# Optimization experiments

Measured on AMD Instinct MI355X. Metric: run time of the kernel, lower is better.

The kernel has to match this reference:

```python
import jax, jax.numpy as jnp
from jax import lax
import numpy as np

B, S, D, H, OUT = 32, 512, 512, 512, 256


def setup_inputs() -> dict:
    key = jax.random.key(0)
    ks = jax.random.split(key, 12)
    sc = 0.05
    return {
        "x": jax.random.normal(ks[0], (B, S, D), jnp.float32),
        "Wf0": jax.random.normal(ks[1], (D + H, H), jnp.float32) * sc,
        "bf0": jax.random.normal(ks[2], (H,), jnp.float32) * sc,
        "Wb0": jax.random.normal(ks[3], (D + H, H), jnp.float32) * sc,
        "bb0": jax.random.normal(ks[4], (H,), jnp.float32) * sc,
        "Wf1": jax.random.normal(ks[5], (3 * H, H), jnp.float32) * sc,
        "bf1": jax.random.normal(ks[6], (H,), jnp.float32) * sc,
        "Wb1": jax.random.normal(ks[7], (3 * H, H), jnp.float32) * sc,
        "bb1": jax.random.normal(ks[8], (H,), jnp.float32) * sc,
        "Wfc": jax.random.normal(ks[9], (2 * H, OUT), jnp.float32) * sc,
        "bfc": jax.random.normal(ks[10], (OUT,), jnp.float32) * sc,
    }


def _direction(xin, W, b, reverse):
    # xin: [B,S,Din]; W: [Din+H, H]. Split into input and hidden parts so the
    # big input projection is one GEMM; only h @ Wh stays in the scan.
    Din = xin.shape[-1]
    Wx, Wh = W[:Din], W[Din:]
    xw = jnp.einsum('bsd,dh->sbh', xin, Wx) + b  # [S,B,H]

    def step(h, xt):
        h = jnp.tanh(xt + h @ Wh)
        return h, h

    h0 = jnp.zeros((xin.shape[0], Wh.shape[1]), xin.dtype)
    h_last, ys = lax.scan(step, h0, xw, reverse=reverse)
    return h_last, jnp.transpose(ys, (1, 0, 2))  # [B,S,H]


def _bilayer(xin, Wf, bf, Wb, bb):
    h_f, out_f = _direction(xin, Wf, bf, reverse=False)
    h_b, out_b = _direction(xin, Wb, bb, reverse=True)
    return jnp.concatenate([out_f, out_b], axis=-1), h_f, h_b


def reference(x, Wf0, bf0, Wb0, bb0, Wf1, bf1, Wb1, bb1, Wfc, bfc):
    y0, hf0, hb0 = _bilayer(x, Wf0, bf0, Wb0, bb0)
    y1, hf1, hb1 = _bilayer(y0, Wf1, bf1, Wb1, bb1)
    seq_repr = jnp.concatenate([hf1, hb1], axis=-1)  # [B, 2H]
    logits = seq_repr @ Wfc + bfc
    final_hf = jnp.stack([hf0, hf1])  # [L,B,H]
    final_hb = jnp.stack([hb0, hb1])
    return logits, final_hf, final_hb
```

## Files before the change

kernel.cpp:

```cpp
#include <hip/hip_runtime.h>


typedef unsigned short u16;
typedef unsigned int u32;
typedef __attribute__((ext_vector_type(8))) short short8;
typedef __attribute__((ext_vector_type(4))) float f32x4;
typedef __attribute__((ext_vector_type(2))) unsigned int u32x2;

#define DEV static __device__ __forceinline__

DEV u16 f2bf(float f) {
  u32 u = __builtin_bit_cast(u32, f);
  u = (u + 0x7fffu + ((u >> 16) & 1u)) >> 16;
  return (u16)u;
}
DEV float bf2f(u16 h) { return __builtin_bit_cast(float, ((u32)h) << 16); }

DEV f32x4 MFMA(short8 a, short8 b, f32x4 c) {
  return __builtin_amdgcn_mfma_f32_16x16x32_bf16(a, b, c, 0, 0, 0);
}

DEV float fast_tanh(float x) {
  float e = exp2f(x * 2.885390082f);
  return 1.0f - 2.0f * __builtin_amdgcn_rcpf(e + 1.0f);
}

DEV short8 ld_b128_coh(const u16* p) {
  short8 r;
  asm volatile("global_load_dwordx4 %0, %1, off sc0 sc1" : "=v"(r) : "v"(p) : "memory");
  return r;
}
DEV short8 ld_b128_l2(const u16* p) {
  short8 r;
  asm volatile("global_load_dwordx4 %0, %1, off sc0" : "=v"(r) : "v"(p) : "memory");
  return r;
}
DEV f32x4 ld_f32x4_vm(const float* p) {
  f32x4 r;
  asm volatile("global_load_dwordx4 %0, %1, off" : "=v"(r) : "v"(p) : "memory");
  return r;
}
DEV u32 ld_u32_coh(const u32* p) {
  u32 r;
  asm volatile("global_load_dword %0, %1, off sc0 sc1\n\ts_waitcnt vmcnt(0)"
               : "=v"(r) : "v"(p) : "memory");
  return r;
}
DEV void st_b64_coh(u16* p, u32x2 v) {
  asm volatile("global_store_dwordx2 %0, %1, off sc0 sc1" :: "v"(p), "v"(v) : "memory");
}
DEV void st_b64_l2(u16* p, u32x2 v) {
  asm volatile("global_store_dwordx2 %0, %1, off sc0" :: "v"(p), "v"(v) : "memory");
}
DEV void st_u32_coh(u32* p, u32 v) {
  asm volatile("global_store_dword %0, %1, off sc0 sc1" :: "v"(p), "v"(v) : "memory");
}
DEV void vm_drain() { asm volatile("s_waitcnt vmcnt(0)" ::: "memory"); }

template<bool LOCAL>
DEV u32 tag_poll(u32* p) {
  u32 r; u32 z = 0;
  if (LOCAL)
    asm volatile("global_atomic_add %0, %1, %2, off sc0\n\ts_waitcnt vmcnt(0)"
                 : "=v"(r) : "v"(p), "v"(z) : "memory");
  else
    asm volatile("global_atomic_add %0, %1, %2, off sc0 sc1\n\ts_waitcnt vmcnt(0)"
                 : "=v"(r) : "v"(p), "v"(z) : "memory");
  return r;
}
template<bool LOCAL>
DEV void tag_post(u32* p) {
  u32 one = 1;
  if (LOCAL)
    asm volatile("global_atomic_add %0, %1, off" :: "v"(p), "v"(one) : "memory");
  else
    asm volatile("global_atomic_add %0, %1, off sc1" :: "v"(p), "v"(one) : "memory");
}

constexpr size_t OFF_CNT  = 0;
constexpr size_t OFF_MB   = 1024;
constexpr size_t OFF_WT0F = 32768;
constexpr size_t NE_WT0   = 512 * 1024;
constexpr size_t SZ_WT0   = NE_WT0 * 2 * 2;
constexpr size_t OFF_WT0B = OFF_WT0F + SZ_WT0;
constexpr size_t OFF_WT1F = OFF_WT0B + SZ_WT0;
constexpr size_t NE_WT1   = 512 * 1536;
constexpr size_t SZ_WT1   = NE_WT1 * 2 * 2;
constexpr size_t OFF_WT1B = OFF_WT1F + SZ_WT1;
constexpr size_t OFF_XWF  = OFF_WT1B + SZ_WT1;
constexpr size_t SZ_XW    = 16384ull * 512 * 4;
constexpr size_t OFF_XWB  = OFF_XWF + SZ_XW;
constexpr size_t OFF_Y0   = OFF_XWB + SZ_XW;
constexpr size_t SZ_Y0    = 16384ull * 1024 * 4;
constexpr size_t OFF_H    = OFF_Y0 + SZ_Y0;

DEV void phase_barrier(u32* c, u32 target) {
  __syncthreads();
  if (threadIdx.x == 0) {
    __hip_atomic_fetch_add(c, 1u, __ATOMIC_RELEASE, __HIP_MEMORY_SCOPE_AGENT);
    int spins = 0;
    while (__hip_atomic_load(c, __ATOMIC_RELAXED, __HIP_MEMORY_SCOPE_AGENT) < target) {
      __builtin_amdgcn_s_sleep(32);
      if (++spins > (1 << 20)) break;
    }
    __builtin_amdgcn_fence(__ATOMIC_ACQUIRE, "agent");
  }
  __syncthreads();
}

DEV void proj_phase(const float* __restrict__ A, bool perm, int bpitch, int bkoff, int K,
                    const u16* __restrict__ wfh, const u16* __restrict__ wfl,
                    const u16* __restrict__ wbh, const u16* __restrict__ wbl,
                    const float* __restrict__ biasF, const float* __restrict__ biasB,
                    float* __restrict__ Cf, float* __restrict__ Cb,
                    u16* aHi, u16* aLo, u16* bHi, u16* bLo) {
  const int tid = threadIdx.x;
  const int l = tid & 63, w = tid >> 6;
  const int lr = l & 15, lk = (l >> 4) * 8;
  const int wm = (w >> 1) * 64, wn = (w & 1) * 64;
  for (int t = blockIdx.x; t < 1024; t += 256) {
    const int dir = t >> 9, tile = t & 511;
    const int mbase = (tile >> 2) * 128, nbase = (tile & 3) * 128;
    const u16* bh_src = dir ? wbh : wfh;
    const u16* bl_src = dir ? wbl : wfl;
    const float* bias = dir ? biasB : biasF;
    float* C = dir ? Cb : Cf;
    f32x4 acc[4][4] = {};
    for (int kk = 0; kk < K; kk += 32) {
      {
        const int row = tid >> 1, half = tid & 1;
        const int r = mbase + row;
        const int srcRow = perm ? (((r & 31) << 9) + (r >> 5)) : r;
        const float* ap = A + (size_t)srcRow * K + kk + half * 16;
        f32x4 q0 = *(const f32x4*)(ap + 0);
        f32x4 q1 = *(const f32x4*)(ap + 4);
        f32x4 q2 = *(const f32x4*)(ap + 8);
        f32x4 q3 = *(const f32x4*)(ap + 12);
        short8 h0, l0, h1, l1;
        #pragma unroll
        for (int e = 0; e < 4; ++e) {
          { float v = q0[e]; u16 hv = f2bf(v); h0[e]   = (short)hv; l0[e]   = (short)f2bf(v - bf2f(hv)); }
          { float v = q1[e]; u16 hv = f2bf(v); h0[e+4] = (short)hv; l0[e+4] = (short)f2bf(v - bf2f(hv)); }
          { float v = q2[e]; u16 hv = f2bf(v); h1[e]   = (short)hv; l1[e]   = (short)f2bf(v - bf2f(hv)); }
          { float v = q3[e]; u16 hv = f2bf(v); h1[e+4] = (short)hv; l1[e+4] = (short)f2bf(v - bf2f(hv)); }
        }
        const int o = row * 40 + half * 16;
        *(short8*)&aHi[o] = h0; *(short8*)&aHi[o + 8] = h1;
        *(short8*)&aLo[o] = l0; *(short8*)&aLo[o + 8] = l1;
        const size_t bo = (size_t)(nbase + row) * bpitch + bkoff + kk + half * 16;
        *(short8*)&bHi[o]     = *(const short8*)&bh_src[bo];
        *(short8*)&bHi[o + 8] = *(const short8*)&bh_src[bo + 8];
        *(short8*)&bLo[o]     = *(const short8*)&bl_src[bo];
        *(short8*)&bLo[o + 8] = *(const short8*)&bl_src[bo + 8];
      }
      __syncthreads();
      short8 afh[4], afl[4], bfh[4], bfl[4];
      #pragma unroll
      for (int i = 0; i < 4; ++i) {
        afh[i] = *(short8*)&aHi[(wm + i * 16 + lr) * 40 + lk];
        afl[i] = *(short8*)&aLo[(wm + i * 16 + lr) * 40 + lk];
        bfh[i] = *(short8*)&bHi[(wn + i * 16 + lr) * 40 + lk];
        bfl[i] = *(short8*)&bLo[(wn + i * 16 + lr) * 40 + lk];
      }
      #pragma unroll
      for (int i = 0; i < 4; ++i)
        #pragma unroll
        for (int j = 0; j < 4; ++j) {
          acc[i][j] = MFMA(afh[i], bfh[j], acc[i][j]);
          acc[i][j] = MFMA(afh[i], bfl[j], acc[i][j]);
          acc[i][j] = MFMA(afl[i], bfh[j], acc[i][j]);
        }
      __syncthreads();
    }
    #pragma unroll
    for (int i = 0; i < 4; ++i)
      #pragma unroll
      for (int j = 0; j < 4; ++j) {
        const int gcol = nbase + wn + j * 16 + lr;
        const float bv = bias[gcol];
        #pragma unroll
        for (int rr = 0; rr < 4; ++rr) {
          const int grow = mbase + wm + i * 16 + (l >> 4) * 4 + rr;
          C[(size_t)grow * 512 + gcol] = acc[i][j][rr] + bv;
        }
      }
  }
}

template<bool LOCAL>
DEV void recurrence(bool fwd, const float* __restrict__ xw,
                    const u16* __restrict__ wtHi, const u16* __restrict__ wtLo,
                    int wpitch, int wkoff,
                    u16* __restrict__ hHi, u16* __restrict__ hLo,
                    float* __restrict__ y0, int ycol0,
                    u32* mb, int wgslot, float* red) {
  const int tid = threadIdx.x;
  const int l = tid & 63, w = tid >> 6;
  const int lr = l & 15, lk4 = l >> 4;
  const int c0 = wgslot * 32;
  short8 wfh[2][4], wfl[2][4];
  #pragma unroll
  for (int ct = 0; ct < 2; ++ct)
    #pragma unroll
    for (int ks = 0; ks < 4; ++ks) {
      const size_t o = (size_t)(c0 + ct * 16 + lr) * wpitch + wkoff + w * 128 + ks * 32 + lk4 * 8;
      wfh[ct][ks] = *(const short8*)&wtHi[o];
      wfl[ct][ks] = *(const short8*)&wtLo[o];
    }
  const int frow = (w & 1) * 16 + lr;
  const int fcb  = c0 + (w >> 1) * 16 + lk4 * 4;
  const u32 mySlot = (u32)(wgslot * 4 + w);
  u32* pollp = mb + wgslot * 64 + l;
  int budget = 1 << 22;
  for (int t = 0; t < 512; ++t) {
    const int s = fwd ? t : (511 - t);
    f32x4 xwv = ld_f32x4_vm(xw + (size_t)(s * 32 + frow) * 512 + fcb);
    if (t) {
      for (;;) {
        u32 v = tag_poll<LOCAL>(pollp);
        if (__all((int)(v >= (u32)t))) break;
        if (--budget < 0) break;
      }
    }
    const u16* hh = hHi + (t & 1) * 16384;
    const u16* hl = hLo + (t & 1) * 16384;
    u16* nhh = hHi + ((t & 1) ^ 1) * 16384;
    u16* nhl = hLo + ((t & 1) ^ 1) * 16384;
    short8 hfh0[4], hfl0[4], hfh1[4], hfl1[4];
    #pragma unroll
    for (int g = 0; g < 4; ++g) {
      const int k = w * 128 + g * 32 + lk4 * 8;
      if (LOCAL) {
        hfh0[g] = ld_b128_l2(&hh[lr * 512 + k]);
        hfl0[g] = ld_b128_l2(&hl[lr * 512 + k]);
        hfh1[g] = ld_b128_l2(&hh[(16 + lr) * 512 + k]);
        hfl1[g] = ld_b128_l2(&hl[(16 + lr) * 512 + k]);
      } else {
        hfh0[g] = ld_b128_coh(&hh[lr * 512 + k]);
        hfl0[g] = ld_b128_coh(&hl[lr * 512 + k]);
        hfh1[g] = ld_b128_coh(&hh[(16 + lr) * 512 + k]);
        hfl1[g] = ld_b128_coh(&hl[(16 + lr) * 512 + k]);
      }
    }
    f32x4 acc[2][2] = {};
    #pragma unroll
    for (int g = 0; g < 4; ++g) {
      if (g == 0)      asm volatile("s_waitcnt vmcnt(12)" ::: "memory");
      else if (g == 1) asm volatile("s_waitcnt vmcnt(8)"  ::: "memory");
      else if (g == 2) asm volatile("s_waitcnt vmcnt(4)"  ::: "memory");
      else             asm volatile("s_waitcnt vmcnt(0)"  ::: "memory");
      __builtin_amdgcn_sched_barrier(0);
      #pragma unroll
      for (int ct = 0; ct < 2; ++ct) {
        acc[ct][0] = MFMA(wfh[ct][g], hfh0[g], acc[ct][0]);
        acc[ct][0] = MFMA(wfh[ct][g], hfl0[g], acc[ct][0]);
        acc[ct][0] = MFMA(wfl[ct][g], hfh0[g], acc[ct][0]);
        acc[ct][1] = MFMA(wfh[ct][g], hfh1[g], acc[ct][1]);
        acc[ct][1] = MFMA(wfh[ct][g], hfl1[g], acc[ct][1]);
        acc[ct][1] = MFMA(wfl[ct][g], hfh1[g], acc[ct][1]);
      }
    }
    #pragma unroll
    for (int ct = 0; ct < 2; ++ct)
      #pragma unroll
      for (int rh = 0; rh < 2; ++rh)
        *(f32x4*)&red[((w * 4 + ct * 2 + rh) * 64 + l) * 4] = acc[ct][rh];
    __syncthreads();
    f32x4 fin = xwv;
    #pragma unroll
    for (int wp = 0; wp < 4; ++wp)
      fin += *(const f32x4*)&red[((wp * 4 + w) * 64 + l) * 4];
    f32x4 tv;
    #pragma unroll
    for (int rr = 0; rr < 4; ++rr) tv[rr] = fast_tanh(fin[rr]);
    u32x2 hw, lw;
    {
      u16 hv[4], lv[4];
      #pragma unroll
      for (int i = 0; i < 4; ++i) { hv[i] = f2bf(tv[i]); lv[i] = f2bf(tv[i] - bf2f(hv[i])); }
      hw[0] = (u32)hv[0] | ((u32)hv[1] << 16); hw[1] = (u32)hv[2] | ((u32)hv[3] << 16);
      lw[0] = (u32)lv[0] | ((u32)lv[1] << 16); lw[1] = (u32)lv[2] | ((u32)lv[3] << 16);
    }
    if (LOCAL) {
      st_b64_l2(&nhh[frow * 512 + fcb], hw);
      st_b64_l2(&nhl[frow * 512 + fcb], lw);
    } else {
      st_b64_coh(&nhh[frow * 512 + fcb], hw);
      st_b64_coh(&nhl[frow * 512 + fcb], lw);
    }
    vm_drain();
    if (l < 16) tag_post<LOCAL>(mb + l * 64 + mySlot);
    if (y0)
      *(f32x4*)&y0[(size_t)(s * 32 + frow) * 1024 + ycol0 + fcb] = tv;
  }
}

__global__ void rnn_init(u32* c) {
  #pragma unroll
  for (int i = 0; i < 8; ++i) c[threadIdx.x * 8 + i] = 0;
}

__global__ __launch_bounds__(256, 1) void rnn_main(
    const float* __restrict__ x,
    const float* __restrict__ Wf0, const float* __restrict__ bf0,
    const float* __restrict__ Wb0, const float* __restrict__ bb0,
    const float* __restrict__ Wf1, const float* __restrict__ bf1,
    const float* __restrict__ Wb1, const float* __restrict__ bb1,
    const float* __restrict__ Wfc, const float* __restrict__ bfc,
    float* __restrict__ out, char* __restrict__ ws) {
  __shared__ __align__(16) u16 lds[20480];
  u16* aHi = lds; u16* aLo = lds + 5120; u16* bHi = lds + 10240; u16* bLo = lds + 15360;
  float* red = (float*)lds;
  __shared__ u32 sh_xcd, sh_slot, sh_el;

  u32* cnt = (u32*)(ws + OFF_CNT);
  u32* mbase = (u32*)(ws + OFF_MB);
  u16* wt0f_hi = (u16*)(ws + OFF_WT0F); u16* wt0f_lo = wt0f_hi + NE_WT0;
  u16* wt0b_hi = (u16*)(ws + OFF_WT0B); u16* wt0b_lo = wt0b_hi + NE_WT0;
  u16* wt1f_hi = (u16*)(ws + OFF_WT1F); u16* wt1f_lo = wt1f_hi + NE_WT1;
  u16* wt1b_hi = (u16*)(ws + OFF_WT1B); u16* wt1b_lo = wt1b_hi + NE_WT1;
  float* xwf = (float*)(ws + OFF_XWF);
  float* xwb = (float*)(ws + OFF_XWB);
  float* y0  = (float*)(ws + OFF_Y0);
  u16* hb = (u16*)(ws + OFF_H);

  const int gtid = blockIdx.x * 256 + threadIdx.x;
  const int bid = blockIdx.x;

  if (threadIdx.x == 0) {
    u32 xcd;
    asm volatile("s_getreg_b32 %0, hwreg(HW_REG_XCC_ID)" : "=s"(xcd));
    xcd &= 7u;
    sh_xcd = xcd;
    sh_slot = __hip_atomic_fetch_add(&cnt[128 + xcd], 1u, __ATOMIC_RELAXED,
                                     __HIP_MEMORY_SCOPE_AGENT);
  }
  __syncthreads();
  const u32 myXcd = sh_xcd, mySlotIdx = sh_slot;

  for (u32 j = gtid; j < (u32)NE_WT0; j += 65536u) {
    const u32 n = j >> 10, r = j & 1023;
    float v = Wf0[(size_t)r * 512 + n];
    u16 hv = f2bf(v); wt0f_hi[j] = hv; wt0f_lo[j] = f2bf(v - bf2f(hv));
    v = Wb0[(size_t)r * 512 + n];
    hv = f2bf(v); wt0b_hi[j] = hv; wt0b_lo[j] = f2bf(v - bf2f(hv));
  }
  for (u32 j = gtid; j < (u32)NE_WT1; j += 65536u) {
    const u32 n = j / 1536u, r = j - n * 1536u;
    float v = Wf1[(size_t)r * 512 + n];
    u16 hv = f2bf(v); wt1f_hi[j] = hv; wt1f_lo[j] = f2bf(v - bf2f(hv));
    v = Wb1[(size_t)r * 512 + n];
    hv = f2bf(v); wt1b_hi[j] = hv; wt1b_lo[j] = f2bf(v - bf2f(hv));
  }
  for (u32 j = gtid; j < 131072u; j += 65536u) ((u32*)hb)[j] = 0;

  u32 ep = 0;
  phase_barrier(cnt, (++ep) * 256);

  if (bid == 0 && threadIdx.x == 0) {
    u32 cv[8];
    for (int i = 0; i < 8; ++i) cv[i] = ld_u32_coh(&cnt[128 + i]);
    int fwdX = 0;
    for (int i = 1; i < 8; ++i) if (cv[i] > cv[fwdX]) fwdX = i;
    int bwdX = (fwdX == 0) ? 1 : 0;
    for (int i = 0; i < 8; ++i) if (i != fwdX && cv[i] > cv[bwdX]) bwdX = i;
    u32 ok = (cv[fwdX] >= 16 && cv[bwdX] >= 16) ? 1u : 0u;
    st_u32_coh(&cnt[160], (u32)fwdX | ((u32)bwdX << 4) | (ok << 8));
    vm_drain();
  }
  phase_barrier(cnt, (++ep) * 256);
  if (threadIdx.x == 0) sh_el = ld_u32_coh(&cnt[160]);
  __syncthreads();
  const u32 el = sh_el;
  const int fwdX = (int)(el & 15), bwdX = (int)((el >> 4) & 15);
  const bool useLocal = ((el >> 8) & 1) != 0;

  bool rf, rb; int slot;
  if (useLocal) {
    rf = ((int)myXcd == fwdX) && (mySlotIdx < 16);
    rb = ((int)myXcd == bwdX) && (mySlotIdx < 16);
    slot = (int)mySlotIdx;
  } else {
    rf = bid < 16;
    rb = bid >= 16 && bid < 32;
    slot = bid & 15;
  }

  proj_phase(x, true, 1024, 0, 512, wt0f_hi, wt0f_lo, wt0b_hi, wt0b_lo,
             bf0, bb0, xwf, xwb, aHi, aLo, bHi, bLo);
  phase_barrier(cnt, (++ep) * 256);

  if (rf) {
    if (useLocal) recurrence<true >(true,  xwf, wt0f_hi, wt0f_lo, 1024, 512,
                    hb + 0 * 65536, hb + 0 * 65536 + 32768, y0, 0,   mbase,        slot, red);
    else          recurrence<false>(true,  xwf, wt0f_hi, wt0f_lo, 1024, 512,
                    hb + 0 * 65536, hb + 0 * 65536 + 32768, y0, 0,   mbase,        slot, red);
  } else if (rb) {
    if (useLocal) recurrence<true >(false, xwb, wt0b_hi, wt0b_lo, 1024, 512,
                    hb + 1 * 65536, hb + 1 * 65536 + 32768, y0, 512, mbase + 1024, slot, red);
    else          recurrence<false>(false, xwb, wt0b_hi, wt0b_lo, 1024, 512,
                    hb + 1 * 65536, hb + 1 * 65536 + 32768, y0, 512, mbase + 1024, slot, red);
  }
  phase_barrier(cnt, (++ep) * 256);

  proj_phase(y0, false, 1536, 0, 1024, wt1f_hi, wt1f_lo, wt1b_hi, wt1b_lo,
             bf1, bb1, xwf, xwb, aHi, aLo, bHi, bLo);
  phase_barrier(cnt, (++ep) * 256);

  if (rf) {
    if (useLocal) recurrence<true >(true,  xwf, wt1f_hi, wt1f_lo, 1536, 1024,
                    hb + 2 * 65536, hb + 2 * 65536 + 32768, nullptr, 0, mbase + 2048, slot, red);
    else          recurrence<false>(true,  xwf, wt1f_hi, wt1f_lo, 1536, 1024,
                    hb + 2 * 65536, hb + 2 * 65536 + 32768, nullptr, 0, mbase + 2048, slot, red);
  } else if (rb) {
    if (useLocal) recurrence<true >(false, xwb, wt1b_hi, wt1b_lo, 1536, 1024,
                    hb + 3 * 65536, hb + 3 * 65536 + 32768, nullptr, 0, mbase + 3072, slot, red);
    else          recurrence<false>(false, xwb, wt1b_hi, wt1b_lo, 1536, 1024,
                    hb + 3 * 65536, hb + 3 * 65536 + 32768, nullptr, 0, mbase + 3072, slot, red);
  }
  phase_barrier(cnt, (++ep) * 256);

  {
    const int i = gtid;
    const int dl = i >> 14, idx = i & 16383;
    const u16* hh = hb + dl * 65536;
    const u16* hl = hh + 32768;
    const float v = bf2f(hh[idx]) + bf2f(hl[idx]);
    const int base = 8192 + ((dl & 1) ? 32768 : 0) + ((dl >> 1) ? 16384 : 0);
    out[base + idx] = v;
  }
  if (bid < 32) {
    const int gid = gtid;
    const int b = gid >> 8, o = gid & 255;
    const u16* f1h = hb + 2 * 65536; const u16* f1l = f1h + 32768;
    const u16* b1h = hb + 3 * 65536; const u16* b1l = b1h + 32768;
    float a = bfc[o];
    for (int k = 0; k < 512; ++k)
      a += (bf2f(f1h[b * 512 + k]) + bf2f(f1l[b * 512 + k])) * Wfc[(size_t)k * 256 + o];
    for (int k = 0; k < 512; ++k)
      a += (bf2f(b1h[b * 512 + k]) + bf2f(b1l[b * 512 + k])) * Wfc[(size_t)(512 + k) * 256 + o];
    out[gid] = a;
  }
}

extern "C" void kernel_launch(void* const* d_in, const int* in_sizes, int n_in,
                              void* d_out, int out_size, void* d_ws, size_t ws_size,
                              hipStream_t stream) {
  (void)in_sizes; (void)n_in; (void)out_size; (void)ws_size;
  const float* x   = (const float*)d_in[0];
  const float* Wf0 = (const float*)d_in[1];
  const float* bf0 = (const float*)d_in[2];
  const float* Wb0 = (const float*)d_in[3];
  const float* bb0 = (const float*)d_in[4];
  const float* Wf1 = (const float*)d_in[5];
  const float* bf1 = (const float*)d_in[6];
  const float* Wb1 = (const float*)d_in[7];
  const float* bb1 = (const float*)d_in[8];
  const float* Wfc = (const float*)d_in[9];
  const float* bfc = (const float*)d_in[10];
  rnn_init<<<1, 1024, 0, stream>>>((u32*)d_ws);
  rnn_main<<<256, 256, 0, stream>>>(x, Wf0, bf0, Wb0, bb0, Wf1, bf1, Wb1, bb1,
                                    Wfc, bfc, (float*)d_out, (char*)d_ws);
}
```

Before: 3.881 ms.

## Halve recurrence workgroups per direction, doubling columns owned by each

Each recurrence workgroup now owns 64 hidden columns instead of 32, so each direction uses 8 workgroups instead of 16. The mailbox polling, tag posting and XCD-locality threshold are all updated to match. This cuts the number of participants in the per-step cross-workgroup handshake, which is meant to lower synchronisation latency per time step. In exchange each workgroup does twice the MFMA work, holds twice as many weight fragments in registers and writes twice the output. The grid barrier also backs off to longer sleeps after a few spins.

```diff
diff --git a/kernel.cpp b/kernel.cpp
--- a/kernel.cpp
+++ b/kernel.cpp
@@ -100,7 +100,8 @@
     __hip_atomic_fetch_add(c, 1u, __ATOMIC_RELEASE, __HIP_MEMORY_SCOPE_AGENT);
     int spins = 0;
     while (__hip_atomic_load(c, __ATOMIC_RELAXED, __HIP_MEMORY_SCOPE_AGENT) < target) {
-      __builtin_amdgcn_s_sleep(32);
+      if (spins < 16) __builtin_amdgcn_s_sleep(32);
+      else { __builtin_amdgcn_s_sleep(127); __builtin_amdgcn_s_sleep(127); }
       if (++spins > (1 << 20)) break;
     }
     __builtin_amdgcn_fence(__ATOMIC_ACQUIRE, "agent");
@@ -197,10 +198,10 @@
   const int tid = threadIdx.x;
   const int l = tid & 63, w = tid >> 6;
   const int lr = l & 15, lk4 = l >> 4;
-  const int c0 = wgslot * 32;
-  short8 wfh[2][4], wfl[2][4];
+  const int c0 = wgslot * 64;
+  short8 wfh[4][4], wfl[4][4];
   #pragma unroll
-  for (int ct = 0; ct < 2; ++ct)
+  for (int ct = 0; ct < 4; ++ct)
     #pragma unroll
     for (int ks = 0; ks < 4; ++ks) {
       const size_t o = (size_t)(c0 + ct * 16 + lr) * wpitch + wkoff + w * 128 + ks * 32 + lk4 * 8;
@@ -210,11 +211,13 @@
   const int frow = (w & 1) * 16 + lr;
   const int fcb  = c0 + (w >> 1) * 16 + lk4 * 4;
   const u32 mySlot = (u32)(wgslot * 4 + w);
-  u32* pollp = mb + wgslot * 64 + l;
+  u32* pollp = mb + wgslot * 64 + (l & 31);
   int budget = 1 << 22;
   for (int t = 0; t < 512; ++t) {
     const int s = fwd ? t : (511 - t);
-    f32x4 xwv = ld_f32x4_vm(xw + (size_t)(s * 32 + frow) * 512 + fcb);
+    const float* xwp = xw + (size_t)(s * 32 + frow) * 512 + fcb;
+    f32x4 xwA = ld_f32x4_vm(xwp);
+    f32x4 xwB = ld_f32x4_vm(xwp + 32);
     if (t) {
       for (;;) {
         u32 v = tag_poll<LOCAL>(pollp);
@@ -242,7 +245,7 @@
         hfl1[g] = ld_b128_coh(&hl[(16 + lr) * 512 + k]);
       }
     }
-    f32x4 acc[2][2] = {};
+    f32x4 acc[4][2] = {};
     #pragma unroll
     for (int g = 0; g < 4; ++g) {
       if (g == 0)      asm volatile("s_waitcnt vmcnt(12)" ::: "memory");
@@ -251,7 +254,7 @@
       else             asm volatile("s_waitcnt vmcnt(0)"  ::: "memory");
       __builtin_amdgcn_sched_barrier(0);
       #pragma unroll
-      for (int ct = 0; ct < 2; ++ct) {
+      for (int ct = 0; ct < 4; ++ct) {
         acc[ct][0] = MFMA(wfh[ct][g], hfh0[g], acc[ct][0]);
         acc[ct][0] = MFMA(wfh[ct][g], hfl0[g], acc[ct][0]);
         acc[ct][0] = MFMA(wfl[ct][g], hfh0[g], acc[ct][0]);
@@ -261,37 +264,50 @@
       }
     }
     #pragma unroll
-    for (int ct = 0; ct < 2; ++ct)
+    for (int ct = 0; ct < 4; ++ct)
       #pragma unroll
       for (int rh = 0; rh < 2; ++rh)
-        *(f32x4*)&red[((w * 4 + ct * 2 + rh) * 64 + l) * 4] = acc[ct][rh];
+        *(f32x4*)&red[((w * 8 + ct * 2 + rh) * 64 + l) * 4] = acc[ct][rh];
     __syncthreads();
-    f32x4 fin = xwv;
-    #pragma unroll
-    for (int wp = 0; wp < 4; ++wp)
-      fin += *(const f32x4*)&red[((wp * 4 + w) * 64 + l) * 4];
-    f32x4 tv;
-    #pragma unroll
-    for (int rr = 0; rr < 4; ++rr) tv[rr] = fast_tanh(fin[rr]);
-    u32x2 hw, lw;
+    f32x4 finA = xwA, finB = xwB;
+    #pragma unroll
+    for (int wp = 0; wp < 4; ++wp) {
+      finA += *(const f32x4*)&red[((wp * 8 + w) * 64 + l) * 4];
+      finB += *(const f32x4*)&red[((wp * 8 + w + 4) * 64 + l) * 4];
+    }
+    f32x4 tA, tB;
+    #pragma unroll
+    for (int rr = 0; rr < 4; ++rr) { tA[rr] = fast_tanh(finA[rr]); tB[rr] = fast_tanh(finB[rr]); }
+    u32x2 hwA, lwA, hwB, lwB;
     {
-      u16 hv[4], lv[4];
-      #pragma unroll
-      for (int i = 0; i < 4; ++i) { hv[i] = f2bf(tv[i]); lv[i] = f2bf(tv[i] - bf2f(hv[i])); }
-      hw[0] = (u32)hv[0] | ((u32)hv[1] << 16); hw[1] = (u32)hv[2] | ((u32)hv[3] << 16);
-      lw[0] = (u32)lv[0] | ((u32)lv[1] << 16); lw[1] = (u32)lv[2] | ((u32)lv[3] << 16);
+      u16 hv[8], lv[8];
+      #pragma unroll
+      for (int i = 0; i < 4; ++i) {
+        hv[i] = f2bf(tA[i]); lv[i] = f2bf(tA[i] - bf2f(hv[i]));
+        hv[4 + i] = f2bf(tB[i]); lv[4 + i] = f2bf(tB[i] - bf2f(hv[4 + i]));
+      }
+      hwA[0] = (u32)hv[0] | ((u32)hv[1] << 16); hwA[1] = (u32)hv[2] | ((u32)hv[3] << 16);
+      lwA[0] = (u32)lv[0] | ((u32)lv[1] << 16); lwA[1] = (u32)lv[2] | ((u32)lv[3] << 16);
+      hwB[0] = (u32)hv[4] | ((u32)hv[5] << 16); hwB[1] = (u32)hv[6] | ((u32)hv[7] << 16);
+      lwB[0] = (u32)lv[4] | ((u32)lv[5] << 16); lwB[1] = (u32)lv[6] | ((u32)lv[7] << 16);
     }
     if (LOCAL) {
-      st_b64_l2(&nhh[frow * 512 + fcb], hw);
-      st_b64_l2(&nhl[frow * 512 + fcb], lw);
+      st_b64_l2(&nhh[frow * 512 + fcb], hwA);
+      st_b64_l2(&nhl[frow * 512 + fcb], lwA);
+      st_b64_l2(&nhh[frow * 512 + fcb + 32], hwB);
+      st_b64_l2(&nhl[frow * 512 + fcb + 32], lwB);
     } else {
-      st_b64_coh(&nhh[frow * 512 + fcb], hw);
-      st_b64_coh(&nhl[frow * 512 + fcb], lw);
+      st_b64_coh(&nhh[frow * 512 + fcb], hwA);
+      st_b64_coh(&nhl[frow * 512 + fcb], lwA);
+      st_b64_coh(&nhh[frow * 512 + fcb + 32], hwB);
+      st_b64_coh(&nhl[frow * 512 + fcb + 32], lwB);
     }
     vm_drain();
-    if (l < 16) tag_post<LOCAL>(mb + l * 64 + mySlot);
-    if (y0)
-      *(f32x4*)&y0[(size_t)(s * 32 + frow) * 1024 + ycol0 + fcb] = tv;
+    if (l < 8) tag_post<LOCAL>(mb + l * 64 + mySlot);
+    if (y0) {
+      *(f32x4*)&y0[(size_t)(s * 32 + frow) * 1024 + ycol0 + fcb] = tA;
+      *(f32x4*)&y0[(size_t)(s * 32 + frow) * 1024 + ycol0 + fcb + 32] = tB;
+    }
   }
 }
 
@@ -364,7 +380,7 @@
     for (int i = 1; i < 8; ++i) if (cv[i] > cv[fwdX]) fwdX = i;
     int bwdX = (fwdX == 0) ? 1 : 0;
     for (int i = 0; i < 8; ++i) if (i != fwdX && cv[i] > cv[bwdX]) bwdX = i;
-    u32 ok = (cv[fwdX] >= 16 && cv[bwdX] >= 16) ? 1u : 0u;
+    u32 ok = (cv[fwdX] >= 8 && cv[bwdX] >= 8) ? 1u : 0u;
     st_u32_coh(&cnt[160], (u32)fwdX | ((u32)bwdX << 4) | (ok << 8));
     vm_drain();
   }
@@ -377,13 +393,13 @@
 
   bool rf, rb; int slot;
   if (useLocal) {
-    rf = ((int)myXcd == fwdX) && (mySlotIdx < 16);
-    rb = ((int)myXcd == bwdX) && (mySlotIdx < 16);
+    rf = ((int)myXcd == fwdX) && (mySlotIdx < 8);
+    rb = ((int)myXcd == bwdX) && (mySlotIdx < 8);
     slot = (int)mySlotIdx;
   } else {
-    rf = bid < 16;
-    rb = bid >= 16 && bid < 32;
-    slot = bid & 15;
+    rf = bid < 8;
+    rb = bid >= 8 && bid < 16;
+    slot = bid & 7;
   }
 
   proj_phase(x, true, 1024, 0, 512, wt0f_hi, wt0f_lo, wt0b_hi, wt0b_lo,
```

New measurement: 4.842 ms. 1.25x slower.
